# Performance work log

Measured on AMD Instinct MI355X. Metric: run time of the kernel, lower is better.

The kernel has to match this reference:

```python
import jax, jax.numpy as jnp
from jax import lax
import numpy as np

T, B, I, H, O = 1000, 256, 128, 512, 32
ALPHA = 20.0 / 100.0  # dt / tau
EXC_RATIO = 0.8
SPARSITY = 0.2


def setup_inputs() -> dict:
    key = jax.random.key(0)
    ks = jax.random.split(key, 8)
    x = jax.random.normal(ks[0], (T, B, I), dtype=jnp.float32)
    w_in = jax.random.normal(ks[1], (H, I), dtype=jnp.float32) * (1.0 / np.sqrt(I))
    b_in = jax.random.uniform(ks[2], (H,), dtype=jnp.float32, minval=-1, maxval=1) / np.sqrt(I)
    w_h = jax.random.normal(ks[3], (H, H), dtype=jnp.float32) * (1.0 / np.sqrt(H))
    b_h = jax.random.uniform(ks[4], (H,), dtype=jnp.float32, minval=-1, maxval=1) / np.sqrt(H)
    n_exc = int(H * EXC_RATIO)
    dale = jnp.where(jnp.arange(H) < n_exc, 1.0, -1.0).astype(jnp.float32)
    # sparse mask: rand < sparsity, diagonal forced True
    sp = (jax.random.uniform(ks[5], (H, H)) < SPARSITY).astype(jnp.float32)
    sparse = jnp.maximum(sp, jnp.eye(H, dtype=jnp.float32))
    fc_w = jax.random.normal(ks[6], (O, H), dtype=jnp.float32) * (1.0 / np.sqrt(H))
    fc_b = jax.random.uniform(ks[7], (O,), dtype=jnp.float32, minval=-1, maxval=1) / np.sqrt(H)
    return {"x": x, "w_in": w_in, "b_in": b_in, "w_h": w_h, "b_h": b_h,
            "dale": dale, "sparse": sparse, "fc_w": fc_w, "fc_b": fc_b}


def reference(x, w_in, b_in, w_h, b_h, dale, sparse, fc_w, fc_b):
    alpha = jnp.float32(ALPHA)
    oma = jnp.float32(1.0 - ALPHA)
    # effective recurrent weight: relu(W) * dale (per presynaptic column) * sparse mask
    w_eff = jax.nn.relu(w_h) * dale[None, :] * sparse  # [H, H]
    # precompute input drive for all timesteps: [T, B, H]
    x_drive = jnp.einsum('tbi,hi->tbh', x, w_in) + b_in

    def step(carry, xd_t):
        state, out = carry
        total = xd_t + out @ w_eff.T + b_h  # [B, H]
        state = state * oma + total * alpha
        out = jax.nn.relu(state)
        return (state, out), out

    init = (jnp.zeros((B, H), x.dtype), jnp.zeros((B, H), x.dtype))
    _, rnn_activity = lax.scan(step, init, x_drive)  # [T, B, H]
    out = jnp.einsum('tbh,oh->tbo', rnn_activity, fc_w) + fc_b  # [T, B, O]
    return out, rnn_activity
```

## Files before the change

### kernel.cpp

```cpp
#include <hip/hip_runtime.h>

#define T_STEPS 1000
#define BATCH   256
#define IN_DIM  128
#define HID     512
#define OUT_DIM 32
#define ALPHA_F 0.2f
#define OMA_F   0.8f
#define MAXNNZ  96
#define BDEPTH  20
#define HSLOT   48


__global__ __launch_bounds__(512) void build_rank_kernel(
    const float* __restrict__ w_h, const float* __restrict__ sparse,
    unsigned int* __restrict__ perm, unsigned int* __restrict__ nnzR)
{
    int tid = threadIdx.x;
    __shared__ int cnt_sh[HID];

    const float4* wr4 = (const float4*)(w_h    + tid * HID);
    const float4* sr4 = (const float4*)(sparse + tid * HID);
    int cnt = 0;
    for (int j4 = 0; j4 < HID / 4; j4++) {
        float4 w = wr4[j4];
        float4 s = sr4[j4];
        if (w.x > 0.f && s.x > 0.5f) cnt++;
        if (w.y > 0.f && s.y > 0.5f) cnt++;
        if (w.z > 0.f && s.z > 0.5f) cnt++;
        if (w.w > 0.f && s.w > 0.5f) cnt++;
    }
    int c = min(cnt, MAXNNZ);

    cnt_sh[tid] = c;
    __syncthreads();
    int rank = 0;
    for (int j = 0; j < HID; j++) {
        int cj = cnt_sh[j];
        rank += (cj < c) || (cj == c && j < tid);
    }
    perm[rank] = (unsigned int)tid;
    nnzR[rank] = (unsigned int)c;
}

__global__ __launch_bounds__(64) void fill_kernel(
    const float* __restrict__ w_h, const float* __restrict__ dale,
    const float* __restrict__ sparse,
    const unsigned int* __restrict__ perm, const unsigned int* __restrict__ nnzR,
    float* __restrict__ val_t, unsigned short* __restrict__ idx_t)
{
    int r    = blockIdx.x;
    int lane = threadIdx.x;
    int h = (int)perm[r];
    int c = (int)nnzR[r];

    float*          vout = val_t + r * MAXNNZ;
    unsigned short* iout = idx_t + r * MAXNNZ;

    for (int k = lane; k < MAXNNZ; k += 64)
        if (k >= c) { vout[k] = 0.f; iout[k] = 0; }

    unsigned long long lt = (1ull << lane) - 1ull;
    int pos_base = 0;
#pragma unroll
    for (int ch = 0; ch < 8; ch++) {
        int j = ch * 64 + lane;
        float w = w_h[h * HID + j];
        float s = sparse[h * HID + j];
        bool pred = (w > 0.f) && (s > 0.5f);
        unsigned long long m = __ballot(pred);
        if (pred) {
            int pos = pos_base + (int)__popcll(m & lt);
            if (pos < MAXNNZ) {
                vout[pos] = w * dale[j];
                iout[pos] = (unsigned short)(j * 4);
            }
        }
        pos_base += (int)__popcll(m);
    }
}

__global__ __launch_bounds__(64) void sched_kernel(
    float* __restrict__ val_t, unsigned short* __restrict__ idx_t,
    unsigned int* __restrict__ nnzR)
{
    int w    = blockIdx.x;
    int lane = threadIdx.x;
    int rank = w * 64 + lane;
    int g    = lane >> 5;
    int l32  = lane & 31;

    __shared__ unsigned short entb[64][32][BDEPTH];
    __shared__ unsigned char  cntb[64][32];
    __shared__ unsigned char  outsrc[64][MAXNNZ];
    __shared__ float          vll[64][MAXNNZ];
    __shared__ volatile int   wbuf[2][32];

    int c = (int)nnzR[rank];
    int S = c;
#pragma unroll
    for (int off = 32; off; off >>= 1) S = max(S, __shfl_xor(S, off));

    for (int b = 0; b < 32; b++) cntb[lane][b] = 0;
    for (int e = 0; e < MAXNNZ; e++) {
        vll[lane][e]    = val_t[rank * MAXNNZ + e];
        outsrc[lane][e] = 255;
    }
    unsigned int bm = 0;
    int rem = 0;
    for (int e = 0; e < c; e++) {
        int word = ((int)idx_t[rank * MAXNNZ + e]) >> 2;
        int b = word & 31;
        int k = (int)cntb[lane][b];
        if (k < BDEPTH) {
            entb[lane][b][k] = (unsigned short)((e << 9) | word);
            cntb[lane][b] = (unsigned char)(k + 1);
            bm |= 1u << b;
            rem++;
        }
    }

    for (int s = 0; s < MAXNNZ; s++) {
        if (s < S) {
            unsigned int claimed = 0;
            int myb = -1;
#pragma unroll
            for (int round = 0; round < 2; round++) {
                int prop = -1;
                if (myb < 0 && rem > 0) {
                    unsigned int avail = bm & ~claimed;
                    if (avail) {
                        int rot = (l32 * 7 + s * 3 + round * 11) & 31;
                        unsigned int av2 = (avail >> rot) | (avail << ((32 - rot) & 31));
                        prop = (__ffs(av2) - 1 + rot) & 31;
                    }
                }
                if (prop >= 0) wbuf[g][prop] = lane;
                int won = 0;
                if (prop >= 0 && wbuf[g][prop] == lane) { myb = prop; won = 1; }
                unsigned int cm = won ? (1u << myb) : 0u;
#pragma unroll
                for (int off = 16; off; off >>= 1)
                    cm |= (unsigned int)__shfl_xor((int)cm, off, 32);
                claimed |= cm;
            }
            if (myb < 0 && rem > 0 && rem >= S - s) {
                unsigned int a = bm & ~claimed;
                myb = a ? (__ffs(a) - 1) : (__ffs(bm) - 1);
            }
            if (myb >= 0) {
                int k = (int)cntb[lane][myb] - 1;
                unsigned short pk = entb[lane][myb][k];
                cntb[lane][myb] = (unsigned char)k;
                if (k == 0) bm &= ~(1u << myb);
                outsrc[lane][s] = (unsigned char)(pk >> 9);
                idx_t[rank * MAXNNZ + s] = (unsigned short)((pk & 511) * 4);
                rem--;
            } else {
                unsigned int freeb = ~claimed;
                int pb = freeb ? (__ffs(freeb) - 1) : 0;
                idx_t[rank * MAXNNZ + s] = (unsigned short)(pb * 4);
            }
        } else {
            idx_t[rank * MAXNNZ + s] = 0;
        }
    }
    nnzR[rank] = (unsigned int)S;

    for (int s = 0; s < MAXNNZ; s++) {
        int src = outsrc[lane][s];
        val_t[rank * MAXNNZ + s] = (src == 255) ? 0.f : vll[lane][src];
    }
}

__global__ __launch_bounds__(256) void trans_kernel(
    const float* __restrict__ w_in, const float* __restrict__ fc_w,
    float* __restrict__ w_inT, float* __restrict__ fcT)
{
    int o = blockIdx.x * 256 + threadIdx.x;
    if (o < IN_DIM * HID) {
        int k = o / HID, n = o % HID;
        w_inT[o] = w_in[n * IN_DIM + k];
    } else {
        int o2 = o - IN_DIM * HID;
        if (o2 < HID * OUT_DIM) {
            int k = o2 / OUT_DIM, oo = o2 % OUT_DIM;
            fcT[o2] = fc_w[oo * HID + k];
        }
    }
}

__global__ __launch_bounds__(256, 4) void ingemm_kernel(
    const float* __restrict__ x, const float* __restrict__ w_inT,
    const float* __restrict__ b_in, const float* __restrict__ b_h,
    float* __restrict__ xd)
{
    __shared__ float xl[256 * 33];
    int tid = threadIdx.x;
    int B  = blockIdx.x;
    int r8 = B & 7;
    int tt = B >> 3;
    int nc = tt & 15;
    int aa = tt >> 4;
    int mb = 8 * aa + r8;
    long m0 = (long)mb * 256;
    int n0 = nc * 32;

    float acc[32];
#pragma unroll
    for (int j = 0; j < 32; j++) acc[j] = b_in[n0 + j] + b_h[n0 + j];

    for (int k0 = 0; k0 < IN_DIM; k0 += 32) {
        __syncthreads();
#pragma unroll
        for (int i = 0; i < 8; i++) {
            int f  = tid + i * 256;
            int rr = f >> 3, cc = f & 7;
            float4 v = *(const float4*)(x + (m0 + rr) * IN_DIM + k0 + cc * 4);
            float* d = &xl[rr * 33 + cc * 4];
            d[0] = v.x; d[1] = v.y; d[2] = v.z; d[3] = v.w;
        }
        __syncthreads();
        const float* xrow = &xl[tid * 33];
#pragma unroll
        for (int kk = 0; kk < 32; kk++) {
            float a = xrow[kk];
            const float* wrow = w_inT + (k0 + kk) * HID + n0;
#pragma unroll
            for (int j = 0; j < 32; j++) acc[j] = fmaf(a, wrow[j], acc[j]);
        }
    }
    float* orow = xd + (m0 + tid) * HID + n0;
#pragma unroll
    for (int j = 0; j < 8; j++)
        *(float4*)(orow + j * 4) =
            make_float4(acc[4*j], acc[4*j+1], acc[4*j+2], acc[4*j+3]);
}


#define PAIR2(base, ii)                                              \
    {                                                                \
        unsigned int pk = idp[ii];                                   \
        float g0 = *(const float*)((base) + (pk & 0xffffu));         \
        float g1 = *(const float*)((base) + (pk >> 16));             \
        a0 = fmaf(val[2*(ii)],     g0, a0);                          \
        a1 = fmaf(val[2*(ii) + 1], g1, a1);                          \
    }

#define CHUNK2(base, c)                                              \
    PAIR2(base, 2*(c)+0) PAIR2(base, 2*(c)+1)

__device__ __forceinline__ float sparse_accum(
    const char* base, const float (&val)[HSLOT],
    const unsigned int (&idp)[HSLOT / 2], int nch, float a_init)
{
    float a0 = a_init, a1 = 0.f;
    switch (nch) {
        case 12: CHUNK2(base, 11) [[fallthrough]];
        case 11: CHUNK2(base, 10) [[fallthrough]];
        case 10: CHUNK2(base,  9) [[fallthrough]];
        case  9: CHUNK2(base,  8) [[fallthrough]];
        case  8: CHUNK2(base,  7) [[fallthrough]];
        case  7: CHUNK2(base,  6) [[fallthrough]];
        case  6: CHUNK2(base,  5) [[fallthrough]];
        case  5: CHUNK2(base,  4) [[fallthrough]];
        case  4: CHUNK2(base,  3) [[fallthrough]];
        case  3: CHUNK2(base,  2) [[fallthrough]];
        case  2: CHUNK2(base,  1) [[fallthrough]];
        case  1: CHUNK2(base,  0) break;
        default: break;
    }
    return a0 + a1;
}

__global__ __launch_bounds__(1024) void scan_kernel(
    float* __restrict__ act_g,
    const float* __restrict__ val_t, const unsigned short* __restrict__ idx_t,
    const unsigned int* __restrict__ perm, const unsigned int* __restrict__ nnzR)
{
    int tid = threadIdx.x;
    int r   = tid & 511;
    int isB = tid >> 9;
    int b   = blockIdx.x;
    __shared__ float sbuf[1024];
    __shared__ float pbuf[512];
    sbuf[tid & 1023] = 0.f;

    int S = (int)nnzR[r | 63];
    S = __builtin_amdgcn_readfirstlane(S);
    int nchT = (S + 3) >> 2;
    int nchA = (nchT + 1) >> 1;
    int nch  = isB ? (nchT - nchA) : nchA;
    int base = isB ? (nchA << 2) : 0;

    float        val[HSLOT];
    unsigned int idp[HSLOT / 2];
    {
        const float4* vp = (const float4*)(val_t + r * MAXNNZ + base);
#pragma unroll
        for (int i = 0; i < HSLOT / 4; i++) {
            float4 v = vp[i];
            val[4*i] = v.x; val[4*i+1] = v.y; val[4*i+2] = v.z; val[4*i+3] = v.w;
        }
        const uint2* ip = (const uint2*)(idx_t + r * MAXNNZ + base);
#pragma unroll
        for (int i = 0; i < HSLOT / 4; i++) {
            uint2 u = ip[i];
            idp[2*i] = u.x; idp[2*i+1] = u.y;
        }
    }
    int h = (int)perm[r];

    float state = 0.f;
    int gi = b * HID + h;
    float xdv = 0.f;
    if (!isB) xdv = act_g[gi];
    const char* sb = (const char*)sbuf;
    __syncthreads();

    for (int t = 0; t < T_STEPS; t += 2) {
        {
            float xn = 0.f;
            if (!isB) xn = act_g[gi + BATCH * HID];
            float ap = sparse_accum(sb, val, idp, nch, isB ? 0.f : xdv);
            if (isB) pbuf[r] = ap;
            __syncthreads();
            float act = 0.f;
            if (!isB) {
                float a = ap + pbuf[r];
                state = state * OMA_F + a * ALPHA_F;
                act = fmaxf(state, 0.f);
                sbuf[512 + h] = act;
            }
            __syncthreads();
            if (!isB) act_g[gi] = act;
            gi += BATCH * HID;
            xdv = xn;
        }
        {
            float xn = 0.f;
            if (!isB) {
                int gn = (t < T_STEPS - 2) ? gi + BATCH * HID : gi;
                xn = act_g[gn];
            }
            float ap = sparse_accum(sb + 2048, val, idp, nch, isB ? 0.f : xdv);
            if (isB) pbuf[r] = ap;
            __syncthreads();
            float act = 0.f;
            if (!isB) {
                float a = ap + pbuf[r];
                state = state * OMA_F + a * ALPHA_F;
                act = fmaxf(state, 0.f);
                sbuf[h] = act;
            }
            __syncthreads();
            if (!isB) act_g[gi] = act;
            gi += BATCH * HID;
            xdv = xn;
        }
    }
}

__global__ __launch_bounds__(256, 4) void outgemm_kernel(
    const float* __restrict__ act_g, const float* __restrict__ fcT,
    const float* __restrict__ fc_b, float* __restrict__ out_g)
{
    __shared__ float al[256 * 33];
    int tid = threadIdx.x;
    long m0 = (long)blockIdx.x * 256;

    float acc[32];
#pragma unroll
    for (int o = 0; o < 32; o++) acc[o] = fc_b[o];

    for (int k0 = 0; k0 < HID; k0 += 32) {
        __syncthreads();
#pragma unroll
        for (int i = 0; i < 8; i++) {
            int f  = tid + i * 256;
            int rr = f >> 3, cc = f & 7;
            float4 v = *(const float4*)(act_g + (m0 + rr) * HID + k0 + cc * 4);
            float* d = &al[rr * 33 + cc * 4];
            d[0] = v.x; d[1] = v.y; d[2] = v.z; d[3] = v.w;
        }
        __syncthreads();
        const float* arow = &al[tid * 33];
#pragma unroll
        for (int kk = 0; kk < 32; kk++) {
            float a = arow[kk];
            const float* frow = fcT + (k0 + kk) * OUT_DIM;
#pragma unroll
            for (int o = 0; o < 32; o++) acc[o] = fmaf(a, frow[o], acc[o]);
        }
    }
    float* orow = out_g + (m0 + tid) * OUT_DIM;
#pragma unroll
    for (int j = 0; j < 8; j++)
        *(float4*)(orow + j * 4) =
            make_float4(acc[4*j], acc[4*j+1], acc[4*j+2], acc[4*j+3]);
}

extern "C" void kernel_launch(void* const* d_in, const int* in_sizes, int n_in,
                              void* d_out, int out_size, void* d_ws, size_t ws_size,
                              hipStream_t stream)
{
    const float* x      = (const float*)d_in[0];
    const float* w_in   = (const float*)d_in[1];
    const float* b_in   = (const float*)d_in[2];
    const float* w_h    = (const float*)d_in[3];
    const float* b_h    = (const float*)d_in[4];
    const float* dale   = (const float*)d_in[5];
    const float* sparse = (const float*)d_in[6];
    const float* fc_w   = (const float*)d_in[7];
    const float* fc_b   = (const float*)d_in[8];

    float* out_g = (float*)d_out;
    float* act_g = out_g + (long)T_STEPS * BATCH * OUT_DIM;

    char* ws = (char*)d_ws;
    float*          val_t = (float*)(ws + 0);
    unsigned short* idx_t = (unsigned short*)(ws + 196608);
    unsigned int*   perm  = (unsigned int*)(ws + 294912);
    unsigned int*   nnzR  = (unsigned int*)(ws + 296960);
    float*          w_inT = (float*)(ws + 299008);
    float*          fcT   = (float*)(ws + 561152);

    build_rank_kernel<<<1, 512, 0, stream>>>(w_h, sparse, perm, nnzR);
    fill_kernel<<<HID, 64, 0, stream>>>(w_h, dale, sparse, perm, nnzR, val_t, idx_t);
    sched_kernel<<<8, 64, 0, stream>>>(val_t, idx_t, nnzR);
    trans_kernel<<<320, 256, 0, stream>>>(w_in, fc_w, w_inT, fcT);
    ingemm_kernel<<<16000, 256, 0, stream>>>(x, w_inT, b_in, b_h, act_g);
    scan_kernel<<<256, 1024, 0, stream>>>(act_g, val_t, idx_t, perm, nnzR);
    outgemm_kernel<<<1000, 256, 0, stream>>>(act_g, fcT, fc_b, out_g);
}
```

Measured before the change: 2.063 ms.

## Split row work across half-wavefronts and combine partial sums with a shuffle

Each hidden row's sparse dot product is now split between the two 32-lane halves of one wavefront, instead of between the two 512-thread halves of the block. The partial sums are combined with __shfl_down, so the shared pbuf array and one of the two __syncthreads per timestep go away. This removes a block-wide barrier from every step of the serial recurrence. The global activation store now reads the value back from shared memory after the remaining barrier, which adds an extra LDS read per step.

```diff
diff --git a/kernel.cpp b/kernel.cpp
--- a/kernel.cpp
+++ b/kernel.cpp
@@ -278,20 +278,21 @@
     const float* __restrict__ val_t, const unsigned short* __restrict__ idx_t,
     const unsigned int* __restrict__ perm, const unsigned int* __restrict__ nnzR)
 {
-    int tid = threadIdx.x;
-    int r   = tid & 511;
-    int isB = tid >> 9;
-    int b   = blockIdx.x;
+    int tid  = threadIdx.x;
+    int w    = tid >> 6;
+    int lane = tid & 63;
+    int r    = w * 32 + (lane & 31);
+    int isA  = (lane < 32);
+    int b    = blockIdx.x;
     __shared__ float sbuf[1024];
-    __shared__ float pbuf[512];
     sbuf[tid & 1023] = 0.f;
 
     int S = (int)nnzR[r | 63];
     S = __builtin_amdgcn_readfirstlane(S);
     int nchT = (S + 3) >> 2;
     int nchA = (nchT + 1) >> 1;
-    int nch  = isB ? (nchT - nchA) : nchA;
-    int base = isB ? (nchA << 2) : 0;
+    int nch  = isA ? nchA : (nchT - nchA);
+    int base = isA ? 0 : (nchA << 2);
 
     float        val[HSLOT];
     unsigned int idp[HSLOT / 2];
@@ -314,47 +315,43 @@
     float state = 0.f;
     int gi = b * HID + h;
     float xdv = 0.f;
-    if (!isB) xdv = act_g[gi];
+    if (isA) xdv = act_g[gi];
     const char* sb = (const char*)sbuf;
     __syncthreads();
 
     for (int t = 0; t < T_STEPS; t += 2) {
         {
             float xn = 0.f;
-            if (!isB) xn = act_g[gi + BATCH * HID];
-            float ap = sparse_accum(sb, val, idp, nch, isB ? 0.f : xdv);
-            if (isB) pbuf[r] = ap;
+            if (isA) xn = act_g[gi + BATCH * HID];
+            float ap = sparse_accum(sb, val, idp, nch, isA ? xdv : 0.f);
+            float bp = __shfl_down(ap, 32);
+            if (isA) {
+                float a = ap + bp;
+                state = state * OMA_F + a * ALPHA_F;
+                float act = fmaxf(state, 0.f);
+                sbuf[512 + h] = act;
+            }
             __syncthreads();
-            float act = 0.f;
-            if (!isB) {
-                float a = ap + pbuf[r];
-                state = state * OMA_F + a * ALPHA_F;
-                act = fmaxf(state, 0.f);
-                sbuf[512 + h] = act;
-            }
-            __syncthreads();
-            if (!isB) act_g[gi] = act;
+            if (isA) act_g[gi] = sbuf[512 + h];
             gi += BATCH * HID;
             xdv = xn;
         }
         {
             float xn = 0.f;
-            if (!isB) {
+            if (isA) {
                 int gn = (t < T_STEPS - 2) ? gi + BATCH * HID : gi;
                 xn = act_g[gn];
             }
-            float ap = sparse_accum(sb + 2048, val, idp, nch, isB ? 0.f : xdv);
-            if (isB) pbuf[r] = ap;
+            float ap = sparse_accum(sb + 2048, val, idp, nch, isA ? xdv : 0.f);
+            float bp = __shfl_down(ap, 32);
+            if (isA) {
+                float a = ap + bp;
+                state = state * OMA_F + a * ALPHA_F;
+                float act = fmaxf(state, 0.f);
+                sbuf[h] = act;
+            }
             __syncthreads();
-            float act = 0.f;
-            if (!isB) {
-                float a = ap + pbuf[r];
-                state = state * OMA_F + a * ALPHA_F;
-                act = fmaxf(state, 0.f);
-                sbuf[h] = act;
-            }
-            __syncthreads();
-            if (!isB) act_g[gi] = act;
+            if (isA) act_g[gi] = sbuf[h];
             gi += BATCH * HID;
             xdv = xn;
         }
```

Result: slower. 2.120 ms (+2.8%).
